# Kernel optimization log

Hardware: AMD Instinct MI355X
Metric: run time of the kernel (lower is better)

## Reference

```python
import jax, jax.numpy as jnp
import numpy as np

N_NODES = 100000
N_EDGES = 800000
IN = 128
HID = 128
EMB = 64
OUT = 8
N_GRAPHS = 64


def setup_inputs() -> dict:
    key = jax.random.key(0)
    ks = jax.random.split(key, 12)
    x = jax.random.normal(ks[0], (N_NODES, IN), dtype=jnp.float32)
    edge_index = jax.random.randint(ks[1], (2, N_EDGES), 0, N_NODES, dtype=jnp.int64)
    batch = jnp.sort(jax.random.randint(ks[2], (N_NODES,), 0, N_GRAPHS, dtype=jnp.int64))
    embed = jax.random.normal(ks[3], (N_GRAPHS, EMB), dtype=jnp.float32)
    s_in = 1.0 / np.sqrt(IN).astype(np.float32)
    s_h = 1.0 / np.sqrt(HID).astype(np.float32)
    s_l = 1.0 / np.sqrt(HID + EMB).astype(np.float32)
    return {
        "x": x,
        "edge_index": edge_index,
        "batch": batch,
        "embed": embed,
        # SAGEConv1: out = lin_l(mean_agg) + lin_r(x); bias lives in lin_l
        "W1l": jax.random.normal(ks[4], (HID, IN), dtype=jnp.float32) * s_in,
        "b1l": jnp.zeros((HID,), dtype=jnp.float32),
        "W1r": jax.random.normal(ks[5], (HID, IN), dtype=jnp.float32) * s_in,
        # SAGEConv2
        "W2l": jax.random.normal(ks[6], (HID, HID), dtype=jnp.float32) * s_h,
        "b2l": jnp.zeros((HID,), dtype=jnp.float32),
        "W2r": jax.random.normal(ks[7], (HID, HID), dtype=jnp.float32) * s_h,
        # final Linear(hidden + embed_dim, out)
        "Wlin": jax.random.normal(ks[8], (OUT, HID + EMB), dtype=jnp.float32) * s_l,
        "blin": jnp.zeros((OUT,), dtype=jnp.float32),
    }


def _segment_mean(vals, idx, num_segments):
    # scatter-mean with count clamped to 1 (matches PyG scatter 'mean')
    s = jax.ops.segment_sum(vals, idx, num_segments=num_segments)
    c = jax.ops.segment_sum(jnp.ones((vals.shape[0], 1), vals.dtype), idx,
                            num_segments=num_segments)
    return s / jnp.maximum(c, 1.0)


def reference(x, edge_index, batch, embed, W1l, b1l, W1r, W2l, b2l, W2r, Wlin, blin):
    src, dst = edge_index[0], edge_index[1]

    def sage(h, Wl, bl, Wr):
        # gather source features, mean-aggregate at destination, then linear
        agg = _segment_mean(h[src], dst, N_NODES)          # [N, d]
        return agg @ Wl.T + bl + h @ Wr.T                   # [N, HID]

    h = jax.nn.relu(sage(x, W1l, b1l, W1r))
    h = jax.nn.relu(sage(h, W2l, b2l, W2r))
    pooled = _segment_mean(h, batch, N_GRAPHS)              # [G, HID]
    z = jnp.concatenate([pooled, embed], axis=1)            # [G, HID+EMB]
    return z @ Wlin.T + blin                                # [G, OUT]
```

## Files before the change

kernel.cpp:

```cpp
#include <hip/hip_runtime.h>
#include <stdint.h>

#define FEAT   128
#define GR     64
#define LDA    136
#define NBUCK  256
#define BSHIFT 9

typedef __attribute__((ext_vector_type(8))) short bf8_t;
typedef __attribute__((ext_vector_type(4))) float f4_t;

__device__ inline float bf2f(ushort h){
    union { uint u; float f; } v; v.u = ((uint)h) << 16; return v.f;
}
__device__ inline float bf2f_lo(uint u){
    union { uint u; float f; } v; v.u = u << 16; return v.f;
}
__device__ inline float bf2f_hi(uint u){
    union { uint u; float f; } v; v.u = u & 0xffff0000u; return v.f;
}
__device__ inline ushort f2bf(float f){
    union { float f; uint u; } v; v.f = f;
    uint r = (v.u + 0x7FFFu + ((v.u >> 16) & 1u)) >> 16;
    return (ushort)r;
}

__global__ void k_cast(const float* __restrict__ x, ushort* __restrict__ xb, int n4){
    int i = blockIdx.x * blockDim.x + threadIdx.x;
    if (i >= n4) return;
    float4 v = ((const float4*)x)[i];
    ushort4 o; o.x = f2bf(v.x); o.y = f2bf(v.y); o.z = f2bf(v.z); o.w = f2bf(v.w);
    ((ushort4*)xb)[i] = o;
}

__global__ void k_castw(const float* __restrict__ a0, const float* __restrict__ a1,
                        const float* __restrict__ a2, const float* __restrict__ a3,
                        ushort* __restrict__ o0, ushort* __restrict__ o1,
                        ushort* __restrict__ o2, ushort* __restrict__ o3){
    int i = blockIdx.x * blockDim.x + threadIdx.x;
    int sel = i >> 12, j = i & 4095;
    const float* s = sel == 0 ? a0 : sel == 1 ? a1 : sel == 2 ? a2 : a3;
    ushort*      d = sel == 0 ? o0 : sel == 1 ? o1 : sel == 2 ? o2 : o3;
    float4 v = ((const float4*)s)[j];
    ushort4 o; o.x = f2bf(v.x); o.y = f2bf(v.y); o.z = f2bf(v.z); o.w = f2bf(v.w);
    ((ushort4*)d)[j] = o;
}

__global__ void k_hist(const int* __restrict__ dst, int* __restrict__ bcnt, int E){
    __shared__ int h[NBUCK];
    h[threadIdx.x] = 0;
    __syncthreads();
    int base = blockIdx.x * 4096 + threadIdx.x;
    #pragma unroll
    for (int k = 0; k < 16; k++){
        int e = base + k * 256;
        if (e < E) atomicAdd(&h[dst[e] >> BSHIFT], 1);
    }
    __syncthreads();
    int c = h[threadIdx.x];
    if (c) atomicAdd(&bcnt[threadIdx.x], c);
}

__global__ void k_bscan(const int* __restrict__ bcnt, int* __restrict__ bbase,
                        int* __restrict__ bpos, int* __restrict__ rowp,
                        int* __restrict__ csr, int E, int M){
    __shared__ int sd[NBUCK];
    int t = threadIdx.x;
    int v = bcnt[t];
    sd[t] = v; __syncthreads();
    for (int off = 1; off < NBUCK; off <<= 1){
        int x = (t >= off) ? sd[t - off] : 0;
        __syncthreads();
        sd[t] += x;
        __syncthreads();
    }
    int ex = sd[t] - v;
    bbase[t] = ex;
    bpos[t]  = ex;
    if (t < 8) csr[E + t] = 0;
    if (t == NBUCK - 1){ bbase[NBUCK] = sd[t]; rowp[M] = E; }
}

__global__ __launch_bounds__(256) void k_bucket(const int* __restrict__ src,
                                                const int* __restrict__ dst,
                                                int* __restrict__ bpos,
                                                int2* __restrict__ bp, int E){
    __shared__ int h[NBUCK];
    __shared__ int bb[NBUCK];
    int t = threadIdx.x;
    h[t] = 0;
    __syncthreads();
    int base = blockIdx.x * 4096 + t;
    int bk[16], sv[16], dv[16];
    #pragma unroll
    for (int k = 0; k < 16; k++){
        int e = base + k * 256;
        if (e < E){
            dv[k] = dst[e]; sv[k] = src[e];
            bk[k] = dv[k] >> BSHIFT;
            atomicAdd(&h[bk[k]], 1);
        } else bk[k] = -1;
    }
    __syncthreads();
    int c = h[t];
    bb[t] = c ? atomicAdd(&bpos[t], c) : 0;
    __syncthreads();
    h[t] = 0;
    __syncthreads();
    #pragma unroll
    for (int k = 0; k < 16; k++){
        if (bk[k] >= 0){
            int r = atomicAdd(&h[bk[k]], 1);
            bp[bb[bk[k]] + r] = make_int2(sv[k], dv[k]);
        }
    }
}

__global__ __launch_bounds__(512) void k_csr(const int2* __restrict__ bp,
                                             const int* __restrict__ bbase,
                                             int* __restrict__ rowp,
                                             int* __restrict__ csr, int M){
    __shared__ int cnt[512];
    __shared__ int sd[512];
    int b = blockIdx.x, t = threadIdx.x;
    int nbase = b << BSHIFT;
    int nnodes = min(512, M - nbase);
    int e0 = bbase[b], e1 = bbase[b + 1];
    cnt[t] = 0;
    __syncthreads();
    for (int e = e0 + t; e < e1; e += 512)
        atomicAdd(&cnt[bp[e].y - nbase], 1);
    __syncthreads();
    int v = cnt[t];
    sd[t] = v; __syncthreads();
    for (int off = 1; off < 512; off <<= 1){
        int x = (t >= off) ? sd[t - off] : 0;
        __syncthreads();
        sd[t] += x;
        __syncthreads();
    }
    int ex = sd[t] - v;
    if (t < nnodes) rowp[nbase + t] = e0 + ex;
    cnt[t] = ex;
    __syncthreads();
    for (int e = e0 + t; e < e1; e += 512){
        int2 pr = bp[e];
        int r = atomicAdd(&cnt[pr.y - nbase], 1);
        csr[e0 + r] = pr.x;
    }
}

__global__ void k_agg(const ushort* __restrict__ srcf, const int* __restrict__ rowp,
                      const int* __restrict__ csr, ushort* __restrict__ aggb, int M){
    int node = blockIdx.x * 4 + (threadIdx.x >> 6);
    int lane = threadIdx.x & 63;
    if (node >= M) return;
    int s = rowp[node], e = rowp[node + 1];
    const char* base = (const char*)srcf + (uint)lane * 4u;
    float a0 = 0.f, a1 = 0.f, b0 = 0.f, b1 = 0.f;
    float c0 = 0.f, c1 = 0.f, d0 = 0.f, d1 = 0.f;
    float e0 = 0.f, e1 = 0.f, g0 = 0.f, g1 = 0.f;
    float p0 = 0.f, p1 = 0.f, q0 = 0.f, q1 = 0.f;
    int i = s;
    for (; i + 8 <= e; i += 8){
        int idx[8];
        __builtin_memcpy(idx, csr + i, 32);
        uint v0 = *(const uint*)(base + ((uint)idx[0] << 8));
        uint v1 = *(const uint*)(base + ((uint)idx[1] << 8));
        uint v2 = *(const uint*)(base + ((uint)idx[2] << 8));
        uint v3 = *(const uint*)(base + ((uint)idx[3] << 8));
        uint v4 = *(const uint*)(base + ((uint)idx[4] << 8));
        uint v5 = *(const uint*)(base + ((uint)idx[5] << 8));
        uint v6 = *(const uint*)(base + ((uint)idx[6] << 8));
        uint v7 = *(const uint*)(base + ((uint)idx[7] << 8));
        a0 += bf2f_lo(v0); a1 += bf2f_hi(v0);
        b0 += bf2f_lo(v1); b1 += bf2f_hi(v1);
        c0 += bf2f_lo(v2); c1 += bf2f_hi(v2);
        d0 += bf2f_lo(v3); d1 += bf2f_hi(v3);
        e0 += bf2f_lo(v4); e1 += bf2f_hi(v4);
        g0 += bf2f_lo(v5); g1 += bf2f_hi(v5);
        p0 += bf2f_lo(v6); p1 += bf2f_hi(v6);
        q0 += bf2f_lo(v7); q1 += bf2f_hi(v7);
    }
    if (i + 4 <= e){
        int idx[4];
        __builtin_memcpy(idx, csr + i, 16);
        uint v0 = *(const uint*)(base + ((uint)idx[0] << 8));
        uint v1 = *(const uint*)(base + ((uint)idx[1] << 8));
        uint v2 = *(const uint*)(base + ((uint)idx[2] << 8));
        uint v3 = *(const uint*)(base + ((uint)idx[3] << 8));
        a0 += bf2f_lo(v0); a1 += bf2f_hi(v0);
        b0 += bf2f_lo(v1); b1 += bf2f_hi(v1);
        c0 += bf2f_lo(v2); c1 += bf2f_hi(v2);
        d0 += bf2f_lo(v3); d1 += bf2f_hi(v3);
        i += 4;
    }
    for (; i < e; i++){
        uint v = *(const uint*)(base + ((uint)csr[i] << 8));
        a0 += bf2f_lo(v); a1 += bf2f_hi(v);
    }
    float s0 = ((a0 + b0) + (c0 + d0)) + ((e0 + g0) + (p0 + q0));
    float s1 = ((a1 + b1) + (c1 + d1)) + ((e1 + g1) + (p1 + q1));
    float inv = (e > s) ? 1.0f / (float)(e - s) : 0.f;
    uint o = ((uint)f2bf(s1 * inv) << 16) | (uint)f2bf(s0 * inv);
    *(uint*)(aggb + (size_t)node * FEAT + lane * 2) = o;
}

__global__ __launch_bounds__(256) void k_gemm(
    const ushort* __restrict__ Aagg, const ushort* __restrict__ Aself,
    const ushort* __restrict__ Wl, const ushort* __restrict__ Wr,
    const float* __restrict__ bias, ushort* __restrict__ Hout, int M)
{
    __shared__ ushort As[64 * LDA];
    __shared__ ushort Bs[128 * LDA];
    const int tid  = threadIdx.x;
    const int lane = tid & 63;
    const int wave = tid >> 6;
    const int l15  = lane & 15;
    const int quad = lane >> 4;
    const int m0   = blockIdx.x * 64;

    f4_t acc[8];
    #pragma unroll
    for (int i = 0; i < 8; i++) acc[i] = (f4_t){0.f, 0.f, 0.f, 0.f};

    #pragma unroll
    for (int pass = 0; pass < 2; pass++){
        const ushort* Ap = pass ? Aself : Aagg;
        const ushort* Wp = pass ? Wr    : Wl;
        #pragma unroll
        for (int it = 0; it < 4; it++){
            int idx = (it * 256 + tid) * 8;
            int r = idx >> 7, c = idx & 127;
            int4 v = {0, 0, 0, 0};
            if (m0 + r < M) v = *(const int4*)(Ap + (size_t)(m0 + r) * FEAT + c);
            *(int4*)(&As[r * LDA + c]) = v;
        }
        #pragma unroll
        for (int it = 0; it < 8; it++){
            int idx = (it * 256 + tid) * 8;
            int r = idx >> 7, c = idx & 127;
            *(int4*)(&Bs[r * LDA + c]) = *(const int4*)(Wp + idx);
        }
        __syncthreads();
        const ushort* arow = &As[(wave * 16 + l15) * LDA + quad * 8];
        const ushort* brow = &Bs[l15 * LDA + quad * 8];
        #pragma unroll
        for (int nt = 0; nt < 8; nt++){
            #pragma unroll
            for (int ks = 0; ks < 4; ks++){
                bf8_t a = *(const bf8_t*)(arow + ks * 32);
                bf8_t b = *(const bf8_t*)(brow + nt * 16 * LDA + ks * 32);
                acc[nt] = __builtin_amdgcn_mfma_f32_16x16x32_bf16(a, b, acc[nt], 0, 0, 0);
            }
        }
        __syncthreads();
    }
    #pragma unroll
    for (int nt = 0; nt < 8; nt++){
        int col = nt * 16 + l15;
        float bcol = bias[col];
        #pragma unroll
        for (int reg = 0; reg < 4; reg++){
            int gm = m0 + wave * 16 + quad * 4 + reg;
            if (gm < M){
                float v = acc[nt][reg] + bcol;
                v = v > 0.f ? v : 0.f;
                Hout[(size_t)gm * FEAT + col] = f2bf(v);
            }
        }
    }
}

__global__ void k_pool(const ushort* __restrict__ h, const int* __restrict__ batch,
                       float* __restrict__ pooled, int M){
    int f   = threadIdx.x & 127;
    int sub = threadIdx.x >> 7;
    int n0  = (blockIdx.x * 2 + sub) * 16;
    if (n0 >= M) return;
    int n1 = min(n0 + 16, M);
    int g = batch[n0];
    float s = 0.f;
    int n = n0;
    for (; n + 4 <= n1; n += 4){
        int g0 = batch[n], g1 = batch[n + 1], g2 = batch[n + 2], g3 = batch[n + 3];
        float v0 = bf2f(h[(size_t)n * FEAT + f]);
        float v1 = bf2f(h[(size_t)(n + 1) * FEAT + f]);
        float v2 = bf2f(h[(size_t)(n + 2) * FEAT + f]);
        float v3 = bf2f(h[(size_t)(n + 3) * FEAT + f]);
        if (g0 != g){ atomicAdd(&pooled[g * FEAT + f], s); s = 0.f; g = g0; } s += v0;
        if (g1 != g){ atomicAdd(&pooled[g * FEAT + f], s); s = 0.f; g = g1; } s += v1;
        if (g2 != g){ atomicAdd(&pooled[g * FEAT + f], s); s = 0.f; g = g2; } s += v2;
        if (g3 != g){ atomicAdd(&pooled[g * FEAT + f], s); s = 0.f; g = g3; } s += v3;
    }
    for (; n < n1; n++){
        int gn = batch[n];
        if (gn != g){ atomicAdd(&pooled[g * FEAT + f], s); s = 0.f; g = gn; }
        s += bf2f(h[(size_t)n * FEAT + f]);
    }
    atomicAdd(&pooled[g * FEAT + f], s);
}

__global__ void k_final(const float* __restrict__ pooled, const int* __restrict__ batch,
                        const float* __restrict__ embed, const float* __restrict__ Wlin,
                        const float* __restrict__ blin, float* __restrict__ out, int M){
    int t = threadIdx.x;
    if (t >= GR * 8) return;
    int g = t >> 3, o = t & 7;
    int lo = 0, hi = M;
    while (lo < hi){ int mid = (lo + hi) >> 1; if (batch[mid] < g) lo = mid + 1; else hi = mid; }
    int s0 = lo;
    lo = s0; hi = M;
    while (lo < hi){ int mid = (lo + hi) >> 1; if (batch[mid] < g + 1) lo = mid + 1; else hi = mid; }
    int c = lo - s0;
    float inv = (c > 0) ? 1.0f / (float)c : 0.f;
    float acc = blin[o];
    const float* wr = Wlin + o * (FEAT + GR);
    for (int k = 0; k < FEAT; k++) acc += pooled[g * FEAT + k] * inv * wr[k];
    for (int k = 0; k < GR; k++)   acc += embed[g * GR + k] * wr[FEAT + k];
    out[g * 8 + o] = acc;
}

extern "C" void kernel_launch(void* const* d_in, const int* in_sizes, int n_in,
                              void* d_out, int out_size, void* d_ws, size_t ws_size,
                              hipStream_t stream)
{
    const float* x     = (const float*)d_in[0];
    const int*   eidx  = (const int*)d_in[1];
    const int*   batch = (const int*)d_in[2];
    const float* embed = (const float*)d_in[3];
    const float* W1l   = (const float*)d_in[4];
    const float* b1l   = (const float*)d_in[5];
    const float* W1r   = (const float*)d_in[6];
    const float* W2l   = (const float*)d_in[7];
    const float* b2l   = (const float*)d_in[8];
    const float* W2r   = (const float*)d_in[9];
    const float* Wlin  = (const float*)d_in[10];
    const float* blin  = (const float*)d_in[11];
    float* out = (float*)d_out;

    const int M = in_sizes[0] / FEAT;
    const int E = in_sizes[1] / 2;
    const int* src = eidx;
    const int* dst = eidx + E;

    char* w = (char*)d_ws;
    size_t off = 0;
    auto alloc = [&](size_t sz){ void* p = w + off; off = (off + sz + 255) & ~(size_t)255; return p; };
    ushort* xb     = (ushort*)alloc((size_t)M * FEAT * 2);
    ushort* aggb   = (ushort*)alloc((size_t)M * FEAT * 2);
    ushort* h1b    = (ushort*)alloc((size_t)M * FEAT * 2);
    int*    rowp   = (int*)alloc((size_t)(M + 1) * 4);
    int*    csr    = (int*)alloc((size_t)(E + 8) * 4);
    int*    bcnt   = (int*)alloc(NBUCK * 4);
    int*    bbase  = (int*)alloc((NBUCK + 1) * 4);
    int*    bpos   = (int*)alloc(NBUCK * 4);
    float*  pooled = (float*)alloc((size_t)GR * FEAT * 4);
    ushort* w1lb   = (ushort*)alloc((size_t)FEAT * FEAT * 2);
    ushort* w1rb   = (ushort*)alloc((size_t)FEAT * FEAT * 2);
    ushort* w2lb   = (ushort*)alloc((size_t)FEAT * FEAT * 2);
    ushort* w2rb   = (ushort*)alloc((size_t)FEAT * FEAT * 2);
    int2*   bp     = (int2*)aggb;
    ushort* h2b    = xb;

    hipMemsetAsync(bcnt, 0, NBUCK * 4, stream);
    hipMemsetAsync(pooled, 0, (size_t)GR * FEAT * 4, stream);

    const int nb   = (M + 511) >> BSHIFT;
    const int ebk  = (E + 4095) / 4096;
    k_cast  <<<(M * FEAT / 4 + 255) / 256, 256, 0, stream>>>(x, xb, M * FEAT / 4);
    k_castw <<<64, 256, 0, stream>>>(W1l, W1r, W2l, W2r, w1lb, w1rb, w2lb, w2rb);
    k_hist  <<<ebk, 256, 0, stream>>>(dst, bcnt, E);
    k_bscan <<<1, NBUCK, 0, stream>>>(bcnt, bbase, bpos, rowp, csr, E, M);
    k_bucket<<<ebk, 256, 0, stream>>>(src, dst, bpos, bp, E);
    k_csr   <<<nb, 512, 0, stream>>>(bp, bbase, rowp, csr, M);
    k_agg   <<<(M + 3) / 4, 256, 0, stream>>>(xb, rowp, csr, aggb, M);
    k_gemm  <<<(M + 63) / 64, 256, 0, stream>>>(aggb, xb, w1lb, w1rb, b1l, h1b, M);
    k_agg   <<<(M + 3) / 4, 256, 0, stream>>>(h1b, rowp, csr, aggb, M);
    k_gemm  <<<(M + 63) / 64, 256, 0, stream>>>(aggb, h1b, w2lb, w2rb, b2l, h2b, M);
    k_pool  <<<(M + 31) / 32, 256, 0, stream>>>(h2b, batch, pooled, M);
    k_final <<<1, 512, 0, stream>>>(pooled, batch, embed, Wlin, blin, out, M);
}
```

Baseline: 327.1 us.

## Fuse neighbor mean aggregation into SAGE GEMM kernel via shared memory

Merges the separate gather-aggregate kernel and the MFMA GEMM kernel into one k_sage kernel. Each wave aggregates its 16 rows directly into the shared-memory A tile, so the bf16 aggregate buffer is never written to or read back from global memory, and two launches per layer are removed. The cost is lower parallelism during the latency-bound gather phase: there are now 1563 blocks that each process 16 nodes serially per wave, where before there was one wave per node with far more waves in flight. The bp buffer now gets its own workspace allocation because it no longer aliases the removed aggregate buffer.

```diff
diff --git a/kernel.cpp b/kernel.cpp
--- a/kernel.cpp
+++ b/kernel.cpp
@@ -150,66 +150,11 @@
     }
 }
 
-__global__ void k_agg(const ushort* __restrict__ srcf, const int* __restrict__ rowp,
-                      const int* __restrict__ csr, ushort* __restrict__ aggb, int M){
-    int node = blockIdx.x * 4 + (threadIdx.x >> 6);
-    int lane = threadIdx.x & 63;
-    if (node >= M) return;
-    int s = rowp[node], e = rowp[node + 1];
-    const char* base = (const char*)srcf + (uint)lane * 4u;
-    float a0 = 0.f, a1 = 0.f, b0 = 0.f, b1 = 0.f;
-    float c0 = 0.f, c1 = 0.f, d0 = 0.f, d1 = 0.f;
-    float e0 = 0.f, e1 = 0.f, g0 = 0.f, g1 = 0.f;
-    float p0 = 0.f, p1 = 0.f, q0 = 0.f, q1 = 0.f;
-    int i = s;
-    for (; i + 8 <= e; i += 8){
-        int idx[8];
-        __builtin_memcpy(idx, csr + i, 32);
-        uint v0 = *(const uint*)(base + ((uint)idx[0] << 8));
-        uint v1 = *(const uint*)(base + ((uint)idx[1] << 8));
-        uint v2 = *(const uint*)(base + ((uint)idx[2] << 8));
-        uint v3 = *(const uint*)(base + ((uint)idx[3] << 8));
-        uint v4 = *(const uint*)(base + ((uint)idx[4] << 8));
-        uint v5 = *(const uint*)(base + ((uint)idx[5] << 8));
-        uint v6 = *(const uint*)(base + ((uint)idx[6] << 8));
-        uint v7 = *(const uint*)(base + ((uint)idx[7] << 8));
-        a0 += bf2f_lo(v0); a1 += bf2f_hi(v0);
-        b0 += bf2f_lo(v1); b1 += bf2f_hi(v1);
-        c0 += bf2f_lo(v2); c1 += bf2f_hi(v2);
-        d0 += bf2f_lo(v3); d1 += bf2f_hi(v3);
-        e0 += bf2f_lo(v4); e1 += bf2f_hi(v4);
-        g0 += bf2f_lo(v5); g1 += bf2f_hi(v5);
-        p0 += bf2f_lo(v6); p1 += bf2f_hi(v6);
-        q0 += bf2f_lo(v7); q1 += bf2f_hi(v7);
-    }
-    if (i + 4 <= e){
-        int idx[4];
-        __builtin_memcpy(idx, csr + i, 16);
-        uint v0 = *(const uint*)(base + ((uint)idx[0] << 8));
-        uint v1 = *(const uint*)(base + ((uint)idx[1] << 8));
-        uint v2 = *(const uint*)(base + ((uint)idx[2] << 8));
-        uint v3 = *(const uint*)(base + ((uint)idx[3] << 8));
-        a0 += bf2f_lo(v0); a1 += bf2f_hi(v0);
-        b0 += bf2f_lo(v1); b1 += bf2f_hi(v1);
-        c0 += bf2f_lo(v2); c1 += bf2f_hi(v2);
-        d0 += bf2f_lo(v3); d1 += bf2f_hi(v3);
-        i += 4;
-    }
-    for (; i < e; i++){
-        uint v = *(const uint*)(base + ((uint)csr[i] << 8));
-        a0 += bf2f_lo(v); a1 += bf2f_hi(v);
-    }
-    float s0 = ((a0 + b0) + (c0 + d0)) + ((e0 + g0) + (p0 + q0));
-    float s1 = ((a1 + b1) + (c1 + d1)) + ((e1 + g1) + (p1 + q1));
-    float inv = (e > s) ? 1.0f / (float)(e - s) : 0.f;
-    uint o = ((uint)f2bf(s1 * inv) << 16) | (uint)f2bf(s0 * inv);
-    *(uint*)(aggb + (size_t)node * FEAT + lane * 2) = o;
-}
-
-__global__ __launch_bounds__(256) void k_gemm(
-    const ushort* __restrict__ Aagg, const ushort* __restrict__ Aself,
-    const ushort* __restrict__ Wl, const ushort* __restrict__ Wr,
-    const float* __restrict__ bias, ushort* __restrict__ Hout, int M)
+__global__ __launch_bounds__(256) void k_sage(
+    const ushort* __restrict__ feat, const int* __restrict__ rowp,
+    const int* __restrict__ csr, const ushort* __restrict__ Wl,
+    const ushort* __restrict__ Wr, const float* __restrict__ bias,
+    ushort* __restrict__ Hout, int M)
 {
     __shared__ ushort As[64 * LDA];
     __shared__ ushort Bs[128 * LDA];
@@ -220,29 +165,77 @@
     const int quad = lane >> 4;
     const int m0   = blockIdx.x * 64;
 
+    #pragma unroll
+    for (int it = 0; it < 8; it++){
+        int idx = (it * 256 + tid) * 8;
+        int r = idx >> 7, c = idx & 127;
+        *(int4*)(&Bs[r * LDA + c]) = *(const int4*)(Wl + idx);
+    }
+
+    const char* gbase = (const char*)feat + (uint)lane * 4u;
+    #pragma unroll 1
+    for (int ni = 0; ni < 16; ni++){
+        int r = wave * 16 + ni;
+        int node = m0 + r;
+        uint o = 0;
+        if (node < M){
+            int s = rowp[node], e = rowp[node + 1];
+            float a0 = 0.f, a1 = 0.f, b0 = 0.f, b1 = 0.f;
+            float c0 = 0.f, c1 = 0.f, d0 = 0.f, d1 = 0.f;
+            float e0 = 0.f, e1 = 0.f, g0 = 0.f, g1 = 0.f;
+            float p0 = 0.f, p1 = 0.f, q0 = 0.f, q1 = 0.f;
+            int i = s;
+            for (; i + 8 <= e; i += 8){
+                int idx[8];
+                __builtin_memcpy(idx, csr + i, 32);
+                uint v0 = *(const uint*)(gbase + ((uint)idx[0] << 8));
+                uint v1 = *(const uint*)(gbase + ((uint)idx[1] << 8));
+                uint v2 = *(const uint*)(gbase + ((uint)idx[2] << 8));
+                uint v3 = *(const uint*)(gbase + ((uint)idx[3] << 8));
+                uint v4 = *(const uint*)(gbase + ((uint)idx[4] << 8));
+                uint v5 = *(const uint*)(gbase + ((uint)idx[5] << 8));
+                uint v6 = *(const uint*)(gbase + ((uint)idx[6] << 8));
+                uint v7 = *(const uint*)(gbase + ((uint)idx[7] << 8));
+                a0 += bf2f_lo(v0); a1 += bf2f_hi(v0);
+                b0 += bf2f_lo(v1); b1 += bf2f_hi(v1);
+                c0 += bf2f_lo(v2); c1 += bf2f_hi(v2);
+                d0 += bf2f_lo(v3); d1 += bf2f_hi(v3);
+                e0 += bf2f_lo(v4); e1 += bf2f_hi(v4);
+                g0 += bf2f_lo(v5); g1 += bf2f_hi(v5);
+                p0 += bf2f_lo(v6); p1 += bf2f_hi(v6);
+                q0 += bf2f_lo(v7); q1 += bf2f_hi(v7);
+            }
+            if (i + 4 <= e){
+                int idx[4];
+                __builtin_memcpy(idx, csr + i, 16);
+                uint v0 = *(const uint*)(gbase + ((uint)idx[0] << 8));
+                uint v1 = *(const uint*)(gbase + ((uint)idx[1] << 8));
+                uint v2 = *(const uint*)(gbase + ((uint)idx[2] << 8));
+                uint v3 = *(const uint*)(gbase + ((uint)idx[3] << 8));
+                a0 += bf2f_lo(v0); a1 += bf2f_hi(v0);
+                b0 += bf2f_lo(v1); b1 += bf2f_hi(v1);
+                c0 += bf2f_lo(v2); c1 += bf2f_hi(v2);
+                d0 += bf2f_lo(v3); d1 += bf2f_hi(v3);
+                i += 4;
+            }
+            for (; i < e; i++){
+                uint v = *(const uint*)(gbase + ((uint)csr[i] << 8));
+                a0 += bf2f_lo(v); a1 += bf2f_hi(v);
+            }
+            float s0 = ((a0 + b0) + (c0 + d0)) + ((e0 + g0) + (p0 + q0));
+            float s1 = ((a1 + b1) + (c1 + d1)) + ((e1 + g1) + (p1 + q1));
+            float inv = (e > s) ? 1.0f / (float)(e - s) : 0.f;
+            o = ((uint)f2bf(s1 * inv) << 16) | (uint)f2bf(s0 * inv);
+        }
+        *(uint*)(&As[r * LDA + lane * 2]) = o;
+    }
+    __syncthreads();
+
     f4_t acc[8];
     #pragma unroll
     for (int i = 0; i < 8; i++) acc[i] = (f4_t){0.f, 0.f, 0.f, 0.f};
 
-    #pragma unroll
-    for (int pass = 0; pass < 2; pass++){
-        const ushort* Ap = pass ? Aself : Aagg;
-        const ushort* Wp = pass ? Wr    : Wl;
-        #pragma unroll
-        for (int it = 0; it < 4; it++){
-            int idx = (it * 256 + tid) * 8;
-            int r = idx >> 7, c = idx & 127;
-            int4 v = {0, 0, 0, 0};
-            if (m0 + r < M) v = *(const int4*)(Ap + (size_t)(m0 + r) * FEAT + c);
-            *(int4*)(&As[r * LDA + c]) = v;
-        }
-        #pragma unroll
-        for (int it = 0; it < 8; it++){
-            int idx = (it * 256 + tid) * 8;
-            int r = idx >> 7, c = idx & 127;
-            *(int4*)(&Bs[r * LDA + c]) = *(const int4*)(Wp + idx);
-        }
-        __syncthreads();
+    {
         const ushort* arow = &As[(wave * 16 + l15) * LDA + quad * 8];
         const ushort* brow = &Bs[l15 * LDA + quad * 8];
         #pragma unroll
@@ -254,8 +247,39 @@
                 acc[nt] = __builtin_amdgcn_mfma_f32_16x16x32_bf16(a, b, acc[nt], 0, 0, 0);
             }
         }
-        __syncthreads();
-    }
+    }
+    __syncthreads();
+
+    #pragma unroll
+    for (int it = 0; it < 4; it++){
+        int idx = (it * 256 + tid) * 8;
+        int r = idx >> 7, c = idx & 127;
+        int4 v = {0, 0, 0, 0};
+        if (m0 + r < M) v = *(const int4*)(feat + (size_t)(m0 + r) * FEAT + c);
+        *(int4*)(&As[r * LDA + c]) = v;
+    }
+    #pragma unroll
+    for (int it = 0; it < 8; it++){
+        int idx = (it * 256 + tid) * 8;
+        int r = idx >> 7, c = idx & 127;
+        *(int4*)(&Bs[r * LDA + c]) = *(const int4*)(Wr + idx);
+    }
+    __syncthreads();
+
+    {
+        const ushort* arow = &As[(wave * 16 + l15) * LDA + quad * 8];
+        const ushort* brow = &Bs[l15 * LDA + quad * 8];
+        #pragma unroll
+        for (int nt = 0; nt < 8; nt++){
+            #pragma unroll
+            for (int ks = 0; ks < 4; ks++){
+                bf8_t a = *(const bf8_t*)(arow + ks * 32);
+                bf8_t b = *(const bf8_t*)(brow + nt * 16 * LDA + ks * 32);
+                acc[nt] = __builtin_amdgcn_mfma_f32_16x16x32_bf16(a, b, acc[nt], 0, 0, 0);
+            }
+        }
+    }
+
     #pragma unroll
     for (int nt = 0; nt < 8; nt++){
         int col = nt * 16 + l15;
@@ -348,8 +372,8 @@
     size_t off = 0;
     auto alloc = [&](size_t sz){ void* p = w + off; off = (off + sz + 255) & ~(size_t)255; return p; };
     ushort* xb     = (ushort*)alloc((size_t)M * FEAT * 2);
-    ushort* aggb   = (ushort*)alloc((size_t)M * FEAT * 2);
     ushort* h1b    = (ushort*)alloc((size_t)M * FEAT * 2);
+    int2*   bp     = (int2*)alloc((size_t)E * 8);
     int*    rowp   = (int*)alloc((size_t)(M + 1) * 4);
     int*    csr    = (int*)alloc((size_t)(E + 8) * 4);
     int*    bcnt   = (int*)alloc(NBUCK * 4);
@@ -360,7 +384,6 @@
     ushort* w1rb   = (ushort*)alloc((size_t)FEAT * FEAT * 2);
     ushort* w2lb   = (ushort*)alloc((size_t)FEAT * FEAT * 2);
     ushort* w2rb   = (ushort*)alloc((size_t)FEAT * FEAT * 2);
-    int2*   bp     = (int2*)aggb;
     ushort* h2b    = xb;
 
     hipMemsetAsync(bcnt, 0, NBUCK * 4, stream);
@@ -374,10 +397,8 @@
     k_bscan <<<1, NBUCK, 0, stream>>>(bcnt, bbase, bpos, rowp, csr, E, M);
     k_bucket<<<ebk, 256, 0, stream>>>(src, dst, bpos, bp, E);
     k_csr   <<<nb, 512, 0, stream>>>(bp, bbase, rowp, csr, M);
-    k_agg   <<<(M + 3) / 4, 256, 0, stream>>>(xb, rowp, csr, aggb, M);
-    k_gemm  <<<(M + 63) / 64, 256, 0, stream>>>(aggb, xb, w1lb, w1rb, b1l, h1b, M);
-    k_agg   <<<(M + 3) / 4, 256, 0, stream>>>(h1b, rowp, csr, aggb, M);
-    k_gemm  <<<(M + 63) / 64, 256, 0, stream>>>(aggb, h1b, w2lb, w2rb, b2l, h2b, M);
+    k_sage  <<<(M + 63) / 64, 256, 0, stream>>>(xb,  rowp, csr, w1lb, w1rb, b1l, h1b, M);
+    k_sage  <<<(M + 63) / 64, 256, 0, stream>>>(h1b, rowp, csr, w2lb, w2rb, b2l, h2b, M);
     k_pool  <<<(M + 31) / 32, 256, 0, stream>>>(h2b, batch, pooled, M);
     k_final <<<1, 512, 0, stream>>>(pooled, batch, embed, Wlin, blin, out, M);
 }
```

New measurement: 418.9 us. +28.0%, slower.
